# Kernel optimization log

Measured on AMD Instinct MI355X. Metric: run time of the kernel, lower is better.

The kernel has to match this reference:

```python
import jax, jax.numpy as jnp
import numpy as np

S, N, F, H, O = 64, 4096, 32, 64, 2  # seq_len, n_nodes, nfeat, nhid, nout


def setup_inputs() -> dict:
    key = jax.random.key(0)
    ks = jax.random.split(key, 8)
    sc = 0.02
    return {
        "x": jax.random.normal(ks[0], (S, N, F), jnp.float32),
        "adj": jax.random.uniform(ks[1], (N, N), jnp.float32) / N,  # dense normalized-ish adjacency
        "W1": jax.random.normal(ks[2], (F, H), jnp.float32) * sc,
        "b1": jnp.zeros((H,), jnp.float32),
        "W2": jax.random.normal(ks[3], (H, O), jnp.float32) * sc,
        "b2": jnp.zeros((O,), jnp.float32),
        "Wih0": jax.random.normal(ks[4], (3 * H, O * N), jnp.float32) * sc,
        "Whh0": jax.random.normal(ks[5], (3 * H, H), jnp.float32) * sc,
        "bih0": jnp.zeros((3 * H,), jnp.float32),
        "bhh0": jnp.zeros((3 * H,), jnp.float32),
        "Wih1": jax.random.normal(ks[6], (3 * H, H), jnp.float32) * sc,
        "Whh1": jax.random.normal(ks[7], (3 * H, H), jnp.float32) * sc,
        "bih1": jnp.zeros((3 * H,), jnp.float32),
        "bhh1": jnp.zeros((3 * H,), jnp.float32),
    }


def _gru_layer(xs, Wih, Whh, bih, bhh):
    # xs: (S, B, in); PyTorch GRU cell semantics, h0 = 0
    B = xs.shape[1]
    h0 = jnp.zeros((B, Whh.shape[1]), xs.dtype)

    def step(h, x_t):
        gi = x_t @ Wih.T + bih            # (B, 3H)
        gh = h @ Whh.T + bhh              # (B, 3H)
        ir, iz, inn = jnp.split(gi, 3, axis=-1)
        hr, hz, hn = jnp.split(gh, 3, axis=-1)
        r = jax.nn.sigmoid(ir + hr)
        z = jax.nn.sigmoid(iz + hz)
        n = jnp.tanh(inn + r * hn)
        h_new = (1.0 - z) * n + z * h
        return h_new, h_new

    hT, ys = jax.lax.scan(step, h0, xs)
    return ys, hT


def reference(x, adj, W1, b1, W2, b2, Wih0, Whh0, bih0, bhh0, Wih1, Whh1, bih1, bhh1):
    # GCN per timestep (vectorized over time): adj @ (x @ W) + b, relu, adj @ (. @ W2) + b2, log_softmax
    # dropout inactive (eval mode)
    support = jnp.einsum('snf,fh->snh', x, W1) + b1          # (S, N, H)
    h = jnp.einsum('ij,sjh->sih', adj, support)              # (S, N, H)
    h = jax.nn.relu(h)
    support2 = jnp.einsum('snh,ho->sno', h, W2) + b2         # (S, N, O)
    g = jnp.einsum('ij,sjo->sio', adj, support2)             # (S, N, O)
    logp = jax.nn.log_softmax(g, axis=-1)                    # dim=1 of (N, O) per node
    rnn_in = logp.reshape(S, 1, N * O)                       # batch = 1 (torch.stack construction)
    ys0, h0T = _gru_layer(rnn_in, Wih0, Whh0, bih0, bhh0)
    ys1, h1T = _gru_layer(ys0, Wih1, Whh1, bih1, bhh1)
    hn = jnp.stack([h0T, h1T])                               # (n_layers, 1, H)
    return ys1, hn
```

## Files before the change

### kernel.cpp

```cpp
#include <hip/hip_runtime.h>
#include <stdint.h>

#define SS 64
#define NN 4096
#define FF 32
#define HH 64
#define OO 2
#define G3 192

typedef float f32x4 __attribute__((ext_vector_type(4)));
typedef short bf16x8 __attribute__((ext_vector_type(8)));
typedef unsigned short u16x8 __attribute__((ext_vector_type(8)));

#define AS1 __attribute__((address_space(1)))
#define AS3 __attribute__((address_space(3)))

__device__ __forceinline__ unsigned short f2bf(float f) {
  union { float f; uint32_t u; } v; v.f = f;
  uint32_t u = v.u;
  uint32_t r = (u + 0x7FFFu + ((u >> 16) & 1u)) >> 16;
  return (unsigned short)r;
}
__device__ __forceinline__ float bf2f(unsigned short s) {
  union { uint32_t u; float f; } v; v.u = ((uint32_t)s) << 16;
  return v.f;
}
__device__ __forceinline__ unsigned char f2e4m3(float x) {
  float a = fabsf(x);
  unsigned s = (x < 0.f) ? 0x80u : 0u;
  if (a >= 448.f) return (unsigned char)(s | 0x7E);
  if (a < 0.015625f) {
    int q = (int)rintf(a * 512.f);
    return (unsigned char)(s | (unsigned)q);
  }
  union { float f; uint32_t u; } v; v.f = a;
  uint32_t b = v.u + 0x7FFFFu + ((v.u >> 20) & 1u);
  int e = (int)(b >> 23) - 127;
  if (e > 8) return (unsigned char)(s | 0x7E);
  return (unsigned char)(s | (unsigned)(((e + 7) << 3) | ((b >> 20) & 7u)));
}

__global__ __launch_bounds__(256) void k_prep(const float* __restrict__ adj,
                                              unsigned short* __restrict__ adjb,
                                              unsigned char* __restrict__ adj8,
                                              float* __restrict__ rowsum,
                                              const float* __restrict__ x,
                                              unsigned char* __restrict__ Xt8) {
  __shared__ float xl[64][33];
  __shared__ float ps[4];
  int tid = threadIdx.x;
  if (blockIdx.x < 4096) {
    int row = blockIdx.x;
    const float4* src = (const float4*)(adj + (size_t)row * 4096);
    ushort4* dst = (ushort4*)(adjb + (size_t)row * 4096);
    uchar4* dst8 = (uchar4*)(adj8 + (size_t)row * 4096);
    float sum = 0.f;
    #pragma unroll
    for (int q = 0; q < 4; ++q) {
      int idx = q * 256 + tid;
      float4 v = src[idx];
      ushort4 r;
      r.x = f2bf(v.x); r.y = f2bf(v.y); r.z = f2bf(v.z); r.w = f2bf(v.w);
      dst[idx] = r;
      uchar4 r8;
      r8.x = f2e4m3(v.x * 4096.f); r8.y = f2e4m3(v.y * 4096.f);
      r8.z = f2e4m3(v.z * 4096.f); r8.w = f2e4m3(v.w * 4096.f);
      dst8[idx] = r8;
      sum += (v.x + v.y) + (v.z + v.w);
    }
    #pragma unroll
    for (int off = 1; off < 64; off <<= 1) sum += __shfl_xor(sum, off);
    if ((tid & 63) == 0) ps[tid >> 6] = sum;
    __syncthreads();
    if (tid == 0) rowsum[row] = (ps[0] + ps[1]) + (ps[2] + ps[3]);
    return;
  }
  int bs = blockIdx.x - 4096;
  int s = bs >> 6, jb = (bs & 63) << 6;
  const float4* xg = (const float4*)(x + ((size_t)s * NN + jb) * FF);
  #pragma unroll
  for (int ii = 0; ii < 2; ++ii) {
    int idx = tid + ii * 256;
    float4 v = xg[idx];
    int j = idx >> 3, f = (idx & 7) << 2;
    xl[j][f] = v.x; xl[j][f + 1] = v.y; xl[j][f + 2] = v.z; xl[j][f + 3] = v.w;
  }
  __syncthreads();
  int f = tid >> 3, jc = tid & 7;
  unsigned int lo = 0, hi = 0;
  #pragma unroll
  for (int jj = 0; jj < 4; ++jj) lo |= ((unsigned int)f2e4m3(xl[jc * 8 + jj][f])) << (jj * 8);
  #pragma unroll
  for (int jj = 0; jj < 4; ++jj) hi |= ((unsigned int)f2e4m3(xl[jc * 8 + 4 + jj][f])) << (jj * 8);
  uint2 ov; ov.x = lo; ov.y = hi;
  *(uint2*)(Xt8 + (size_t)(s * 32 + f) * 4096 + jb + jc * 8) = ov;
}

#define SBAR()   asm volatile("s_barrier" ::: "memory")
#define VMC9()   asm volatile("s_waitcnt vmcnt(9)" ::: "memory")
#define VMC6()   asm volatile("s_waitcnt vmcnt(6)" ::: "memory")
#define VMC3()   asm volatile("s_waitcnt vmcnt(3)" ::: "memory")
#define VMC0()   asm volatile("s_waitcnt vmcnt(0)" ::: "memory")

__global__ __launch_bounds__(512, 2) void k_gemmAX(
    const unsigned char* __restrict__ A8,
    const unsigned char* __restrict__ B8,
    const float* __restrict__ rowsum,
    const float* __restrict__ W1f,
    const float* __restrict__ b1f,
    const float* __restrict__ W2f,
    const float* __restrict__ b2f,
    unsigned short* __restrict__ B2t) {
  __shared__ __align__(16) char lds[122880];
  __shared__ __align__(16) unsigned short w1t[64 * 40];
  __shared__ float w2l[128];
  __shared__ float b1l[64];
  __shared__ float b2l[2];
  const int tid = threadIdx.x;
  const int wid = tid >> 6, l = tid & 63;
  const int wr2 = wid >> 2, wc2 = wid & 3;
  const int lc = l & 15, lq = l >> 4;

  {
    float4 v = ((const float4*)W1f)[tid];
    int f = tid >> 4, h = (tid & 15) * 4;
    w1t[(h + 0) * 40 + f] = f2bf(v.x);
    w1t[(h + 1) * 40 + f] = f2bf(v.y);
    w1t[(h + 2) * 40 + f] = f2bf(v.z);
    w1t[(h + 3) * 40 + f] = f2bf(v.w);
  }
  if (tid < 32) *(float4*)&w2l[tid * 4] = ((const float4*)W2f)[tid];
  if (tid < 16) *(float4*)&b1l[tid * 4] = ((const float4*)b1f)[tid];
  if (tid < 2) b2l[tid] = b2f[tid];
  __syncthreads();

  int bid = blockIdx.x;
  int swz = (bid & 7) * 32 + (bid >> 3);
  const int i0 = (swz >> 3) * 128;
  const int c0 = (swz & 7) * 256;

  const int aBase = (wr2 * 64 + lc) * 64;
  const int bBase = 8192 + (wc2 * 64 + lc) * 64;
  const int aswz = (lc & 3) ^ ((lc >> 2) & 3);
  const int ck0 = ((((lq >> 1)) ^ aswz) << 4) + (lq & 1) * 8;
  const int ck1 = (((2 + (lq >> 1)) ^ aswz) << 4) + (lq & 1) * 8;

  const int srow = wid * 16 + (l >> 2);
  const int sswz = (srow & 3) ^ ((srow >> 2) & 3);
  const int scol = (((l & 3) ^ sswz) << 4);
  const char* gA = (const char*)A8 + (size_t)(i0 + srow) * 4096 + scol;
  const char* gB = (const char*)B8 + (size_t)(c0 + srow) * 4096 + scol;
  char* ldsW = (char*)lds + wid * 1024;
  const char* ldsR = (const char*)lds;

  f32x4 acc[4][4];
  #pragma unroll
  for (int m = 0; m < 4; ++m)
    #pragma unroll
    for (int n = 0; n < 4; ++n) acc[m][n] = {0.f, 0.f, 0.f, 0.f};

  long afr[4][2], bfr[4][2];

#define STAGE3(KT, BOFS) do {                                                        \
    __builtin_amdgcn_global_load_lds((const AS1 void*)(gA + (KT) * 64),              \
        (AS3 void*)(ldsW + (BOFS)), 16, 0, 0);                                       \
    __builtin_amdgcn_global_load_lds((const AS1 void*)(gB + (KT) * 64),              \
        (AS3 void*)(ldsW + (BOFS) + 8192), 16, 0, 0);                                \
    __builtin_amdgcn_global_load_lds((const AS1 void*)(gB + 524288 + (KT) * 64),     \
        (AS3 void*)(ldsW + (BOFS) + 16384), 16, 0, 0);                               \
  } while (0)

#define READ_FR(BOFS) do {                                                           \
    _Pragma("unroll")                                                                \
    for (int _m = 0; _m < 4; ++_m) {                                                 \
      const char* _p = ldsR + (BOFS) + aBase + _m * 1024;                            \
      afr[_m][0] = *(const long*)(_p + ck0);                                         \
      afr[_m][1] = *(const long*)(_p + ck1);                                         \
    }                                                                                \
    _Pragma("unroll")                                                                \
    for (int _n = 0; _n < 4; ++_n) {                                                 \
      const char* _q = ldsR + (BOFS) + bBase + _n * 1024;                            \
      bfr[_n][0] = *(const long*)(_q + ck0);                                         \
      bfr[_n][1] = *(const long*)(_q + ck1);                                         \
    } } while (0)

#define MFMA32() do {                                                                \
    __builtin_amdgcn_s_setprio(1);                                                   \
    _Pragma("unroll")                                                                \
    for (int _kk = 0; _kk < 2; ++_kk)                                                \
      _Pragma("unroll")                                                              \
      for (int _m = 0; _m < 4; ++_m)                                                 \
        _Pragma("unroll")                                                            \
        for (int _n = 0; _n < 4; ++_n)                                               \
          acc[_m][_n] = __builtin_amdgcn_mfma_f32_16x16x32_fp8_fp8(                  \
              afr[_m][_kk], bfr[_n][_kk], acc[_m][_n], 0, 0, 0);                     \
    __builtin_amdgcn_s_setprio(0);                                                   \
  } while (0)

  STAGE3(0, 0);
  STAGE3(1, 24576);
  STAGE3(2, 49152);
  STAGE3(3, 73728);
  VMC9();
  SBAR();

  int bR = 0, bS = 98304;
  for (int kt = 0; kt < 60; ++kt) {
    READ_FR(bR);
    STAGE3(kt + 4, bS);
    MFMA32();
    VMC9();
    SBAR();
    bR = (bR == 98304) ? 0 : bR + 24576;
    bS = (bS == 98304) ? 0 : bS + 24576;
  }
  READ_FR(bR); MFMA32(); VMC6(); SBAR(); bR = (bR == 98304) ? 0 : bR + 24576;
  READ_FR(bR); MFMA32(); VMC3(); SBAR(); bR = (bR == 98304) ? 0 : bR + 24576;
  READ_FR(bR); MFMA32(); VMC0(); SBAR(); bR = (bR == 98304) ? 0 : bR + 24576;
  READ_FR(bR); MFMA32();
  __syncthreads();

  unsigned short* C1L = (unsigned short*)lds;
  {
    const int rb = wr2 * 64 + lq * 4;
    const int cbL = wc2 * 64 + lc;
    #pragma unroll
    for (int m = 0; m < 4; ++m)
      #pragma unroll
      for (int r = 0; r < 4; ++r) {
        const int row = rb + m * 16 + r;
        #pragma unroll
        for (int n = 0; n < 4; ++n)
          C1L[row * 264 + cbL + n * 16] = f2bf(acc[m][n][r] * 0.000244140625f);
      }
  }
  __syncthreads();

  {
    const f32x4 zacc = {0.f, 0.f, 0.f, 0.f};
    bf16x8 bw[4];
    float b1v[4], w2a[4], w2b[4];
    #pragma unroll
    for (int n = 0; n < 4; ++n) {
      const int h = n * 16 + lc;
      bw[n] = *(const bf16x8*)((const char*)w1t + h * 80 + lq * 16);
      b1v[n] = b1l[h];
      w2a[n] = w2l[h * 2];
      w2b[n] = w2l[h * 2 + 1];
    }
    const int rbase = wid * 16 + lq * 4;
    const float4 rs4 = *(const float4*)&rowsum[i0 + rbase];
    const float bo0 = b2l[0], bo1 = b2l[1];
    #pragma unroll
    for (int s = 0; s < 8; ++s) {
      bf16x8 afe = *(const bf16x8*)((const char*)C1L +
                     (wid * 16 + lc) * 528 + s * 64 + lq * 16);
      float o0r[4] = {0.f, 0.f, 0.f, 0.f};
      float o1r[4] = {0.f, 0.f, 0.f, 0.f};
      #pragma unroll
      for (int n = 0; n < 4; ++n) {
        f32x4 hq = __builtin_amdgcn_mfma_f32_16x16x32_bf16(afe, bw[n], zacc, 0, 0, 0);
        #pragma unroll
        for (int r = 0; r < 4; ++r) {
          float hv = hq[r] + rs4[r] * b1v[n];
          hv = hv > 0.f ? hv : 0.f;
          o0r[r] += hv * w2a[n];
          o1r[r] += hv * w2b[n];
        }
      }
      #pragma unroll
      for (int off = 1; off < 16; off <<= 1)
        #pragma unroll
        for (int r = 0; r < 4; ++r) {
          o0r[r] += __shfl_xor(o0r[r], off);
          o1r[r] += __shfl_xor(o1r[r], off);
        }
      if (lc == 0) {
        const int sg = (c0 >> 5) + s;
        #pragma unroll
        for (int r = 0; r < 4; ++r) {
          B2t[(size_t)(sg * 2 + 0) * 4096 + i0 + rbase + r] = f2bf(o0r[r] + bo0);
          B2t[(size_t)(sg * 2 + 1) * 4096 + i0 + rbase + r] = f2bf(o1r[r] + bo1);
        }
      }
    }
  }
}

__device__ __forceinline__ void gemm_core(const unsigned short* __restrict__ A,
                                          const unsigned short* __restrict__ B,
                                          int i0, int c0, int k0base, int ksteps,
                                          f32x4 acc[4][4],
                                          unsigned short* Als, unsigned short* Bls) {
  const int tid = threadIdx.x;
  const int w = tid >> 6, l = tid & 63;
  const int srow = (l >> 2);
  const int scol = (l & 3) * 16;
  for (int kt = 0; kt < ksteps; ++kt) {
    int k0 = k0base + kt * 32;
    #pragma unroll
    for (int q = 0; q < 2; ++q) {
      int r = w * 32 + q * 16 + srow;
      const char* ga = (const char*)(A + (size_t)(i0 + r) * 4096 + k0) + scol;
      __builtin_amdgcn_global_load_lds(
          (const AS1 void*)ga,
          (AS3 void*)((char*)Als + w * 2048 + q * 1024), 16, 0, 0);
      const char* gb = (const char*)(B + (size_t)(c0 + r) * 4096 + k0) + scol;
      __builtin_amdgcn_global_load_lds(
          (const AS1 void*)gb,
          (AS3 void*)((char*)Bls + w * 2048 + q * 1024), 16, 0, 0);
    }
    __syncthreads();
    const int wr = w >> 1, wc = w & 1;
    bf16x8 af[4], bff[4];
    #pragma unroll
    for (int m = 0; m < 4; ++m)
      af[m] = *(const bf16x8*)(Als + (wr * 64 + m * 16 + (l & 15)) * 32 + (l >> 4) * 8);
    #pragma unroll
    for (int n = 0; n < 4; ++n)
      bff[n] = *(const bf16x8*)(Bls + (wc * 64 + n * 16 + (l & 15)) * 32 + (l >> 4) * 8);
    #pragma unroll
    for (int m = 0; m < 4; ++m)
      #pragma unroll
      for (int n = 0; n < 4; ++n)
        acc[m][n] = __builtin_amdgcn_mfma_f32_16x16x32_bf16(af[m], bff[n], acc[m][n], 0, 0, 0);
    __syncthreads();
  }
}

__global__ __launch_bounds__(256) void k_gemm2(const unsigned short* __restrict__ A,
                                               const unsigned short* __restrict__ B,
                                               float* __restrict__ Gp) {
  __shared__ unsigned short Als[128 * 32], Bls[128 * 32];
  int id = blockIdx.x;
  int bi = id & 31, ks = id >> 5;
  int i0 = bi * 128;
  f32x4 acc[4][4];
  #pragma unroll
  for (int m = 0; m < 4; ++m)
    #pragma unroll
    for (int n = 0; n < 4; ++n) acc[m][n] = {0.f, 0.f, 0.f, 0.f};
  gemm_core(A, B, i0, 0, ks * 512, 16, acc, Als, Bls);
  float* outp = Gp + (size_t)ks * 4096 * 128;
  int l = threadIdx.x & 63, w = threadIdx.x >> 6;
  int wr = w >> 1, wc = w & 1;
  int rbase = i0 + wr * 64 + (l >> 4) * 4;
  int cbase = wc * 64 + (l & 15);
  #pragma unroll
  for (int m = 0; m < 4; ++m)
    #pragma unroll
    for (int n = 0; n < 4; ++n)
      #pragma unroll
      for (int r = 0; r < 4; ++r)
        outp[(size_t)(rbase + m * 16 + r) * 128 + cbase + n * 16] = acc[m][n][r];
}

__global__ __launch_bounds__(256) void k_lsm(const float* __restrict__ Gp,
                                             float* __restrict__ Rm) {
  __shared__ float Gacc[32][130];
  int i0 = blockIdx.x * 32;
  int tid = threadIdx.x;
  float4 v[4];
  #pragma unroll
  for (int i = 0; i < 4; ++i) v[i] = {0.f, 0.f, 0.f, 0.f};
  for (int ks = 0; ks < 8; ++ks) {
    const float4* gp4 = ((const float4*)Gp) + (size_t)ks * 131072 + (size_t)i0 * 32;
    #pragma unroll
    for (int i = 0; i < 4; ++i) {
      float4 t = gp4[tid + i * 256];
      v[i].x += t.x; v[i].y += t.y; v[i].z += t.z; v[i].w += t.w;
    }
  }
  #pragma unroll
  for (int i = 0; i < 4; ++i) {
    int f4i = tid + i * 256, row = f4i >> 5, c = (f4i & 31) * 4;
    Gacc[row][c] = v[i].x; Gacc[row][c + 1] = v[i].y;
    Gacc[row][c + 2] = v[i].z; Gacc[row][c + 3] = v[i].w;
  }
  __syncthreads();
  #pragma unroll
  for (int j = 0; j < 8; ++j) {
    int p = j * 256 + tid;
    int ii = p & 31, s = p >> 5;
    float g0 = Gacc[ii][s * 2], g1 = Gacc[ii][s * 2 + 1];
    float m = fmaxf(g0, g1);
    float lse = m + logf(expf(g0 - m) + expf(g1 - m));
    float2 o_; o_.x = g0 - lse; o_.y = g1 - lse;
    *((float2*)(Rm + (size_t)s * 8192 + (size_t)(i0 + ii) * 2)) = o_;
  }
}

__global__ __launch_bounds__(256) void k_gi0(const float* __restrict__ Rm,
                                             const float* __restrict__ Wih0,
                                             float* __restrict__ part) {
  __shared__ float4 Wl[4 * 128];
  int gb = blockIdx.x % 48, ks = blockIdx.x / 48;
  int c0 = ks * 512;
  int tid = threadIdx.x;
  #pragma unroll
  for (int i = 0; i < 2; ++i) {
    int idx = tid + i * 256;
    int g = idx >> 7, c4 = idx & 127;
    Wl[g * 128 + c4] = ((const float4*)(Wih0 + (size_t)(gb * 4 + g) * 8192 + c0))[c4];
  }
  __syncthreads();
  int w = tid >> 6, lane = tid & 63;
  for (int pass = 0; pass < 16; ++pass) {
    int t = pass * 4 + w;
    float a0 = 0.f, a1 = 0.f, a2 = 0.f, a3 = 0.f;
    const float4* rg = (const float4*)(Rm + (size_t)t * 8192 + c0);
    #pragma unroll
    for (int i = 0; i < 2; ++i) {
      int c4 = i * 64 + lane;
      float4 r4 = rg[c4];
      float4 w0 = Wl[c4], w1 = Wl[128 + c4], w2 = Wl[256 + c4], w3 = Wl[384 + c4];
      a0 += r4.x * w0.x + r4.y * w0.y + r4.z * w0.z + r4.w * w0.w;
      a1 += r4.x * w1.x + r4.y * w1.y + r4.z * w1.z + r4.w * w1.w;
      a2 += r4.x * w2.x + r4.y * w2.y + r4.z * w2.z + r4.w * w2.w;
      a3 += r4.x * w3.x + r4.y * w3.y + r4.z * w3.z + r4.w * w3.w;
    }
    #pragma unroll
    for (int off = 1; off < 64; off <<= 1) {
      a0 += __shfl_xor(a0, off);
      a1 += __shfl_xor(a1, off);
      a2 += __shfl_xor(a2, off);
      a3 += __shfl_xor(a3, off);
    }
    if (lane == 0) {
      float4 o_; o_.x = a0; o_.y = a1; o_.z = a2; o_.w = a3;
      *((float4*)(part + ((size_t)ks * 64 + t) * 192 + gb * 4)) = o_;
    }
  }
}

__global__ __launch_bounds__(256) void k_gi0red(const float* __restrict__ part,
                                                const float* __restrict__ bih0,
                                                float* __restrict__ gi0) {
  int idx = blockIdx.x * 256 + threadIdx.x;
  if (idx < 12288) {
    float s_ = bih0[idx % 192];
    for (int ks = 0; ks < 16; ++ks) s_ += part[ks * 12288 + idx];
    gi0[idx] = s_;
  }
}

__device__ __forceinline__ float fsigm(float x) {
  return __builtin_amdgcn_rcpf(1.f + __expf(-x));
}
__device__ __forceinline__ float ftanh(float x) {
  return 1.f - 2.f * __builtin_amdgcn_rcpf(1.f + __expf(2.f * x));
}

__global__ __launch_bounds__(384) void k_gru(const float* __restrict__ gi0,
                                             const float* __restrict__ Whh0,
                                             const float* __restrict__ bhh0,
                                             const float* __restrict__ Wih1,
                                             const float* __restrict__ Whh1,
                                             const float* __restrict__ bih1,
                                             const float* __restrict__ bhh1,
                                             float* __restrict__ out) {
  __shared__ float gil[64][192];
  __shared__ float gout[576];
  __shared__ __align__(16) unsigned short hv[2][64];
  const int tid = threadIdx.x;
  const int w = tid >> 6, l = tid & 63;
  const int matw = w >> 1, half = w & 1;
  const float* Wm = (matw == 0) ? Whh0 : (matw == 1 ? Wih1 : Whh1);
  const int mi = (matw == 2) ? 1 : 0;

  bf16x8 afr[6][2];
  #pragma unroll
  for (int rbi = 0; rbi < 6; ++rbi) {
    int g = (half * 6 + rbi) * 16 + (l & 15);
    #pragma unroll
    for (int kh = 0; kh < 2; ++kh) {
      int k0 = kh * 32 + (l >> 4) * 8;
      const float4* src = (const float4*)(Wm + (size_t)g * 64 + k0);
      float4 v0 = src[0], v1 = src[1];
      bf16x8 a;
      a[0] = (short)f2bf(v0.x); a[1] = (short)f2bf(v0.y);
      a[2] = (short)f2bf(v0.z); a[3] = (short)f2bf(v0.w);
      a[4] = (short)f2bf(v1.x); a[5] = (short)f2bf(v1.y);
      a[6] = (short)f2bf(v1.z); a[7] = (short)f2bf(v1.w);
      afr[rbi][kh] = a;
    }
  }
  {
    float4* gf = (float4*)&gil[0][0];
    const float4* gs = (const float4*)gi0;
    #pragma unroll
    for (int i = 0; i < 8; ++i) gf[i * 384 + tid] = gs[i * 384 + tid];
  }
  if (tid < 128) hv[tid >> 6][tid & 63] = 0;

  float hreg = 0.f;
  float bR = 0.f, bZ = 0.f, bNa = 0.f, bNb = 0.f;
  if (tid < 64) {
    bR = bhh0[tid]; bZ = bhh0[64 + tid]; bNa = bhh0[128 + tid];
  } else if (tid < 128) {
    int g = tid - 64;
    bR = bih1[g] + bhh1[g];
    bZ = bih1[64 + g] + bhh1[64 + g];
    bNa = bih1[128 + g];
    bNb = bhh1[128 + g];
  }
  asm volatile("s_waitcnt lgkmcnt(0)\n\ts_barrier" ::: "memory");

  const int gwb = matw * 192 + half * 96 + (l >> 4) * 4;
  const f32x4 zacc = {0.f, 0.f, 0.f, 0.f};

  for (int i = 0; i <= 64; ++i) {
    bf16x8 b0 = *(const bf16x8*)&hv[mi][(l >> 4) * 8];
    bf16x8 b1 = *(const bf16x8*)&hv[mi][32 + (l >> 4) * 8];
    #pragma unroll
    for (int rbi = 0; rbi < 6; ++rbi) {
      f32x4 a_ = __builtin_amdgcn_mfma_f32_16x16x32_bf16(afr[rbi][0], b0, zacc, 0, 0, 0);
      a_ = __builtin_amdgcn_mfma_f32_16x16x32_bf16(afr[rbi][1], b1, a_, 0, 0, 0);
      if (!(l & 15)) *(f32x4*)&gout[gwb + rbi * 16] = a_;
    }
    asm volatile("s_waitcnt lgkmcnt(0)\n\ts_barrier" ::: "memory");
    if (tid < 64) {
      if (i < 64) {
        float r = fsigm(gil[i][tid] + gout[tid] + bR);
        float z = fsigm(gil[i][64 + tid] + gout[64 + tid] + bZ);
        float n = ftanh(gil[i][128 + tid] + r * (gout[128 + tid] + bNa));
        hreg = (1.f - z) * n + z * hreg;
        hv[0][tid] = f2bf(hreg);
      }
    } else if (tid < 128 && i > 0) {
      int g = tid - 64;
      float r = fsigm(gout[192 + g] + gout[384 + g] + bR);
      float z = fsigm(gout[256 + g] + gout[448 + g] + bZ);
      float n = ftanh((gout[320 + g] + bNa) + r * (gout[512 + g] + bNb));
      hreg = (1.f - z) * n + z * hreg;
      hv[1][g] = f2bf(hreg);
      out[(i - 1) * 64 + g] = hreg;
    }
    asm volatile("s_waitcnt lgkmcnt(0)\n\ts_barrier" ::: "memory");
  }
  if (tid < 64) out[4096 + tid] = hreg;
  else if (tid < 128) out[4096 + 64 + (tid - 64)] = hreg;
}

extern "C" void kernel_launch(void* const* d_in, const int* in_sizes, int n_in,
                              void* d_out, int out_size, void* d_ws, size_t ws_size,
                              hipStream_t stream) {
  const float* x    = (const float*)d_in[0];
  const float* adj  = (const float*)d_in[1];
  const float* W1   = (const float*)d_in[2];
  const float* b1   = (const float*)d_in[3];
  const float* W2   = (const float*)d_in[4];
  const float* b2   = (const float*)d_in[5];
  const float* Wih0 = (const float*)d_in[6];
  const float* Whh0 = (const float*)d_in[7];
  const float* bih0 = (const float*)d_in[8];
  const float* bhh0 = (const float*)d_in[9];
  const float* Wih1 = (const float*)d_in[10];
  const float* Whh1 = (const float*)d_in[11];
  const float* bih1 = (const float*)d_in[12];
  const float* bhh1 = (const float*)d_in[13];
  float* out = (float*)d_out;

  char* ws = (char*)d_ws;
  unsigned short* adjb = (unsigned short*)ws;
  unsigned char* adj8  = (unsigned char*)(ws + 33554432);
  unsigned char* Xt8   = (unsigned char*)(ws + 50331648);
  float* rowsum        = (float*)(ws + 58720256);
  float* Gp            = (float*)(ws + 58736640);
  float* Rm            = (float*)(ws + 75513856);
  float* part          = (float*)(ws + 77611008);
  float* gi0           = (float*)(ws + 78397440);
  unsigned short* B2t  = (unsigned short*)(ws + 78446592);

  k_prep<<<8192, 256, 0, stream>>>(adj, adjb, adj8, rowsum, x, Xt8);
  k_gemmAX<<<256, 512, 0, stream>>>(adj8, Xt8, rowsum, W1, b1, W2, b2, B2t);
  k_gemm2<<<256, 256, 0, stream>>>(adjb, B2t, Gp);
  k_lsm<<<128, 256, 0, stream>>>(Gp, Rm);
  k_gi0<<<768, 256, 0, stream>>>(Rm, Wih0, part);
  k_gi0red<<<48, 256, 0, stream>>>(part, bih0, gi0);
  k_gru<<<1, 384, 0, stream>>>(gi0, Whh0, bhh0, Wih1, Whh1, bih1, bhh1, out);
}
```

Before: 165.5 us.

## Permute FP8 operand layout so MFMA fragments load as 16-byte LDS reads

The FP8 adjacency and transposed-feature buffers are written with their 8-byte K-chunks permuted within each 64-byte group. Each lane's two MFMA k-slices then sit next to each other in LDS. The GEMM can then fetch both slices with one 128-bit LDS read per fragment instead of two 64-bit reads, halving LDS read instructions in the inner loop. The permutation has to match exactly between the producer kernel and the consumer's swizzle, otherwise the K dimension is mismatched.

```diff
diff --git a/kernel.cpp b/kernel.cpp
--- a/kernel.cpp
+++ b/kernel.cpp
@@ -11,6 +11,7 @@
 typedef float f32x4 __attribute__((ext_vector_type(4)));
 typedef short bf16x8 __attribute__((ext_vector_type(8)));
 typedef unsigned short u16x8 __attribute__((ext_vector_type(8)));
+typedef long longx2 __attribute__((ext_vector_type(2)));
 
 #define AS1 __attribute__((address_space(1)))
 #define AS3 __attribute__((address_space(3)))
@@ -65,7 +66,10 @@
       uchar4 r8;
       r8.x = f2e4m3(v.x * 4096.f); r8.y = f2e4m3(v.y * 4096.f);
       r8.z = f2e4m3(v.z * 4096.f); r8.w = f2e4m3(v.w * 4096.f);
-      dst8[idx] = r8;
+      int o8 = (idx >> 1) & 7;
+      int np = ((o8 & 3) << 1) | (o8 >> 2);
+      int nidx = (idx & ~15) | (np << 1) | (idx & 1);
+      dst8[nidx] = r8;
       sum += (v.x + v.y) + (v.z + v.w);
     }
     #pragma unroll
@@ -93,7 +97,8 @@
   #pragma unroll
   for (int jj = 0; jj < 4; ++jj) hi |= ((unsigned int)f2e4m3(xl[jc * 8 + 4 + jj][f])) << (jj * 8);
   uint2 ov; ov.x = lo; ov.y = hi;
-  *(uint2*)(Xt8 + (size_t)(s * 32 + f) * 4096 + jb + jc * 8) = ov;
+  int np = ((jc & 3) << 1) | (jc >> 2);
+  *(uint2*)(Xt8 + (size_t)(s * 32 + f) * 4096 + jb + np * 8) = ov;
 }
 
 #define SBAR()   asm volatile("s_barrier" ::: "memory")
@@ -142,8 +147,7 @@
   const int aBase = (wr2 * 64 + lc) * 64;
   const int bBase = 8192 + (wc2 * 64 + lc) * 64;
   const int aswz = (lc & 3) ^ ((lc >> 2) & 3);
-  const int ck0 = ((((lq >> 1)) ^ aswz) << 4) + (lq & 1) * 8;
-  const int ck1 = (((2 + (lq >> 1)) ^ aswz) << 4) + (lq & 1) * 8;
+  const int ckx = ((lq ^ aswz) << 4);
 
   const int srow = wid * 16 + (l >> 2);
   const int sswz = (srow & 3) ^ ((srow >> 2) & 3);
@@ -159,7 +163,7 @@
     #pragma unroll
     for (int n = 0; n < 4; ++n) acc[m][n] = {0.f, 0.f, 0.f, 0.f};
 
-  long afr[4][2], bfr[4][2];
+  longx2 afq[4], bfq[4];
 
 #define STAGE3(KT, BOFS) do {                                                        \
     __builtin_amdgcn_global_load_lds((const AS1 void*)(gA + (KT) * 64),              \
@@ -172,17 +176,12 @@
 
 #define READ_FR(BOFS) do {                                                           \
     _Pragma("unroll")                                                                \
-    for (int _m = 0; _m < 4; ++_m) {                                                 \
-      const char* _p = ldsR + (BOFS) + aBase + _m * 1024;                            \
-      afr[_m][0] = *(const long*)(_p + ck0);                                         \
-      afr[_m][1] = *(const long*)(_p + ck1);                                         \
-    }                                                                                \
+    for (int _m = 0; _m < 4; ++_m)                                                   \
+      afq[_m] = *(const longx2*)(ldsR + (BOFS) + aBase + _m * 1024 + ckx);           \
     _Pragma("unroll")                                                                \
-    for (int _n = 0; _n < 4; ++_n) {                                                 \
-      const char* _q = ldsR + (BOFS) + bBase + _n * 1024;                            \
-      bfr[_n][0] = *(const long*)(_q + ck0);                                         \
-      bfr[_n][1] = *(const long*)(_q + ck1);                                         \
-    } } while (0)
+    for (int _n = 0; _n < 4; ++_n)                                                   \
+      bfq[_n] = *(const longx2*)(ldsR + (BOFS) + bBase + _n * 1024 + ckx);           \
+  } while (0)
 
 #define MFMA32() do {                                                                \
     __builtin_amdgcn_s_setprio(1);                                                   \
@@ -193,7 +192,7 @@
         _Pragma("unroll")                                                            \
         for (int _n = 0; _n < 4; ++_n)                                               \
           acc[_m][_n] = __builtin_amdgcn_mfma_f32_16x16x32_fp8_fp8(                  \
-              afr[_m][_kk], bfr[_n][_kk], acc[_m][_n], 0, 0, 0);                     \
+              afq[_m][_kk], bfq[_n][_kk], acc[_m][_n], 0, 0, 0);                     \
     __builtin_amdgcn_s_setprio(0);                                                   \
   } while (0)
 
```

Result: faster. 158.6 us (-4.2%).
